# Performance work log

Hardware: AMD Instinct MI355X
Metric: run time of the kernel (lower is better)

The kernel has to match this reference:

```python
import jax, jax.numpy as jnp
import numpy as np

K = 16
BN_EPS = 1e-3  # keras BatchNormalization default epsilon
LRELU_ALPHA = 0.1


def _lrelu(x):
    return jnp.where(x > 0, x, LRELU_ALPHA * x)


def _bn(x, gamma, beta):
    # training-mode batch norm over all axes except the last (channels)
    axes = tuple(range(x.ndim - 1))
    m = jnp.mean(x, axis=axes)
    v = jnp.var(x, axis=axes)
    return gamma * (x - m) * jax.lax.rsqrt(v + BN_EPS) + beta


def setup_inputs() -> dict:
    key = jax.random.key(0)
    ks = jax.random.split(key, 14)
    N, P, Cp, C0 = 32, 1024, 3, 64
    channels = [128, 128, 256]
    inp = {
        "points": jax.random.normal(ks[0], (N, P, Cp), dtype=jnp.float32),
        "features": jax.random.normal(ks[1], (N, P, C0), dtype=jnp.float32),
    }
    # edge-conv 1x1 weights (no bias, with_bn=True); glorot-ish scaling
    c_in = 2 * C0
    for i, c_out in enumerate(channels):
        scale = (2.0 / (c_in + c_out)) ** 0.5
        inp[f"W{i}"] = jax.random.normal(ks[2 + i], (c_in, c_out), dtype=jnp.float32) * scale
        inp[f"g{i}"] = jnp.ones((c_out,), dtype=jnp.float32)
        inp[f"b{i}"] = jnp.zeros((c_out,), dtype=jnp.float32)
        c_in = c_out
    # shortcut 1x1 conv C0 -> channels[-1]
    scale = (2.0 / (C0 + channels[-1])) ** 0.5
    inp["Wsc"] = jax.random.normal(ks[10], (C0, channels[-1]), dtype=jnp.float32) * scale
    inp["gsc"] = jnp.ones((channels[-1],), dtype=jnp.float32)
    inp["bsc"] = jnp.zeros((channels[-1],), dtype=jnp.float32)
    return inp


def reference(points, features, W0, g0, b0, W1, g1, b1, W2, g2, b2, Wsc, gsc, bsc):
    # pairwise squared distance matrix D: (N, P, P)
    r = jnp.sum(points * points, axis=-1)
    D = r[:, :, None] - 2.0 * jnp.einsum("npc,nqc->npq", points, points) + r[:, None, :]
    # kNN indices, excluding self (first neighbor)
    _, idx = jax.lax.top_k(-D, K + 1)
    idx = idx[:, :, 1:]  # (N, P, K)
    # gather neighbor features per batch element -> (N, P, K, C0)
    knn_fts = jax.vmap(lambda f, i: f[i])(features, idx)
    center = jnp.broadcast_to(features[:, :, None, :], knn_fts.shape)
    x = jnp.concatenate([center, knn_fts - center], axis=-1)  # (N, P, K, 2*C0)
    for W, g, b in ((W0, g0, b0), (W1, g1, b1), (W2, g2, b2)):
        x = _lrelu(_bn(jnp.einsum("npkc,cd->npkd", x, W), g, b))
    fts = jnp.mean(x, axis=2)  # average pooling over K -> (N, P, C_out)
    sc = _bn(jnp.einsum("npc,cd->npd", features, Wsc), gsc, bsc)
    return _lrelu(sc + fts)
```

## Files before the change

### kernel.cpp

```cpp
#include <hip/hip_runtime.h>
#include <stdint.h>

typedef __bf16 bf16x8 __attribute__((ext_vector_type(8)));
typedef float f32x4 __attribute__((ext_vector_type(4)));

union FragU { uint4 q; bf16x8 v; };

__device__ __forceinline__ float bf2f(uint32_t h){
  union U{uint32_t u; float f;} x; x.u = h<<16; return x.f;
}
__device__ __forceinline__ uint32_t f2bf(float f){
  union U{float f; uint32_t u;} x; x.f=f;
  return (x.u + 0x7FFFu + ((x.u>>16)&1u)) >> 16;
}
__device__ __forceinline__ float lrelu(float x){ return fmaxf(x, 0.1f*x); }

__global__ __launch_bounds__(256) void knn_kernel(const float* __restrict__ points, int* __restrict__ idx){
  __shared__ float sx[1024], sy[1024], sz[1024];
  __shared__ unsigned long long scand[4][64];
  const int n = blockIdx.y;
  const float* P = points + (size_t)n*1024*3;
  for(int q=threadIdx.x; q<1024; q+=256){
    sx[q]=P[q*3+0]; sy[q]=P[q*3+1]; sz[q]=P[q*3+2];
  }
  __syncthreads();
  const int wv = threadIdx.x>>6;
  const int lane = threadIdx.x & 63;
  const int p = blockIdx.x*4 + wv;
  const double px=sx[p], py=sy[p], pz=sz[p];
  const double rp = px*px+py*py+pz*pz;
  unsigned long long e[16];
  const int prel = p - lane;
  #pragma unroll
  for(int j=0;j<16;j++){
    const int q = lane + j*64;
    double qx=sx[q], qy=sy[q], qz=sz[q];
    double rq = qx*qx+qy*qy+qz*qz;
    double dot = px*qx+py*qy+pz*qz;
    float key = fmaxf((float)((rp+rq) - 2.0*dot), 0.0f);
    if(prel == j*64) key = __builtin_inff();
    e[j] = ((unsigned long long)__float_as_uint(key) << 10) | (unsigned)q;
  }
  unsigned long long h = e[0];
  #pragma unroll
  for(int j=1;j<16;j++) h = (e[j] < h) ? e[j] : h;
  {
    unsigned long long hs = h;
    #pragma unroll
    for(int k=2;k<=64;k<<=1){
      #pragma unroll
      for(int j=32;j>0;j>>=1){
        if(j < k){
          unsigned long long o = __shfl_xor(hs, j);
          const bool keepMax = (((lane & j)!=0) ^ ((lane & k)!=0));
          hs = keepMax ? (hs > o ? hs : o) : (hs < o ? hs : o);
        }
      }
    }
    h = hs;
  }
  const unsigned long long H = __shfl(h, 15);
  int cnt = 0;
  #pragma unroll
  for(int j=0;j<16;j++) cnt += (e[j] <= H) ? 1 : 0;
  int inc = cnt;
  #pragma unroll
  for(int d=1; d<64; d<<=1){
    int t = __shfl_up(inc, d);
    if(lane >= d) inc += t;
  }
  const int m = __shfl(inc, 63);
  const int base = inc - cnt;
  int* op = idx + ((size_t)n*1024 + p)*16;
  if(m <= 64){
    unsigned long long* sc = scand[wv];
    int slot = base;
    #pragma unroll
    for(int j=0;j<16;j++){
      if(e[j] <= H){ sc[slot] = e[j]; slot++; }
    }
    unsigned long long v = (lane < m) ? sc[lane] : ~0ULL;
    #pragma unroll
    for(int k=2;k<=64;k<<=1){
      #pragma unroll
      for(int j=32;j>0;j>>=1){
        if(j < k){
          unsigned long long o = __shfl_xor(v, j);
          const bool keepMax = (((lane & j)!=0) ^ ((lane & k)!=0));
          v = keepMax ? (v > o ? v : o) : (v < o ? v : o);
        }
      }
    }
    if(lane < 16) op[lane] = (int)(v & 1023u);
  } else {
    for(int it=0; it<16; ++it){
      unsigned long long bd = e[0];
      #pragma unroll
      for(int j=1;j<16;j++) bd = (e[j] < bd) ? e[j] : bd;
      unsigned long long pk = bd;
      #pragma unroll
      for(int s=1;s<64;s<<=1){
        unsigned long long o = __shfl_xor(pk, s);
        pk = (o < pk) ? o : pk;
      }
      #pragma unroll
      for(int j=0;j<16;j++) e[j] = (e[j]==pk) ? ~0ULL : e[j];
      if(lane==0) op[it] = (int)(pk & 1023u);
    }
  }
}

__global__ void wprep_kernel(const float* __restrict__ W0, const float* __restrict__ Wsc,
                             const float* __restrict__ W1, const float* __restrict__ W2,
                             uint16_t* __restrict__ Wpp, uint16_t* __restrict__ W1p,
                             uint16_t* __restrict__ W2p){
  const int stride = gridDim.x*blockDim.x;
  const int t0 = blockIdx.x*blockDim.x + threadIdx.x;
  for(int o=t0; o<32768; o+=stride){
    int j=o&7, l=(o>>3)&63, kc=(o>>9)&1, ct=(o>>10)&3, w=o>>12;
    int k = kc*32 + (l>>4)*8 + j;
    int c = w*64 + ct*16 + (l&15);
    float val;
    if(c<128)      val = W0[k*128+c] - W0[(k+64)*128+c];
    else if(c<256) val = W0[(k+64)*128 + (c-128)];
    else           val = Wsc[k*256 + (c-256)];
    Wpp[o] = (uint16_t)f2bf(val);
  }
  for(int o=t0; o<16384; o+=stride){
    int j=o&7, l=(o>>3)&63, kc=(o>>9)&3, ct=(o>>11)&1, w=o>>12;
    int k = kc*32 + (l>>4)*8 + j, c = w*32 + ct*16 + (l&15);
    W1p[o] = (uint16_t)f2bf(W1[k*128+c]);
  }
  for(int o=t0; o<32768; o+=stride){
    int j=o&7, l=(o>>3)&63, kc=(o>>9)&3, ct=(o>>11)&3, w=o>>13;
    int k = kc*32 + (l>>4)*8 + j, c = w*64 + ct*16 + (l&15);
    W2p[o] = (uint16_t)f2bf(W2[k*256+c]);
  }
}

__global__ __launch_bounds__(512) void proj_kernel(const float* __restrict__ feat,
    const uint16_t* __restrict__ Wpp,
    float* __restrict__ F1, float* __restrict__ F2, float* __restrict__ Fsc,
    float* __restrict__ screps){
  __shared__ alignas(16) uint16_t sA[64*64];
  const int b = blockIdx.x;
  const int tid = threadIdx.x;
  {
    const int row = tid>>3, cc = tid&7;
    const float* src = feat + ((size_t)b*64+row)*64 + cc*8;
    const float4 f0 = *(const float4*)(src);
    const float4 f1 = *(const float4*)(src+4);
    uint32_t pk[4] = { f2bf(f0.x)|(f2bf(f0.y)<<16), f2bf(f0.z)|(f2bf(f0.w)<<16),
                       f2bf(f1.x)|(f2bf(f1.y)<<16), f2bf(f1.z)|(f2bf(f1.w)<<16) };
    int bo = row*128 + cc*16; bo ^= (row&7)<<4;
    *(uint4*)((char*)sA + bo) = make_uint4(pk[0],pk[1],pk[2],pk[3]);
  }
  __syncthreads();
  const int w = tid>>6, l = tid&63;
  FragU bfr[4][2];
  #pragma unroll
  for(int ct=0;ct<4;ct++)
    #pragma unroll
    for(int kc=0;kc<2;kc++)
      bfr[ct][kc].q = *(const uint4*)(Wpp + ((size_t)((w*4+ct)*2+kc))*512 + l*8);
  f32x4 acc[4][4] = {};
  #pragma unroll
  for(int rt=0;rt<4;rt++){
    FragU a[2];
    #pragma unroll
    for(int kc=0;kc<2;kc++){
      const int row = rt*16 + (l&15);
      int bo = row*128 + kc*64 + (l>>4)*16; bo ^= (row&7)<<4;
      a[kc].q = *(const uint4*)((const char*)sA + bo);
    }
    #pragma unroll
    for(int ct=0;ct<4;ct++)
      #pragma unroll
      for(int kc=0;kc<2;kc++)
        acc[rt][ct] = __builtin_amdgcn_mfma_f32_16x16x32_bf16(a[kc].v, bfr[ct][kc].v, acc[rt][ct], 0,0,0);
  }
  #pragma unroll
  for(int rt=0;rt<4;rt++){
    #pragma unroll
    for(int ct=0;ct<4;ct++){
      const int c = w*64 + ct*16 + (l&15);
      const int rowg = b*64 + rt*16 + (l>>4)*4;
      #pragma unroll
      for(int reg=0;reg<4;reg++){
        float v = acc[rt][ct][reg];
        if(c < 128)      F1[(size_t)(rowg+reg)*128 + c] = v;
        else if(c < 256) F2[(size_t)(rowg+reg)*128 + (c-128)] = v;
        else             Fsc[(size_t)(rowg+reg)*256 + (c-256)] = v;
      }
    }
  }
  if(w>=4){
    #pragma unroll
    for(int ct=0;ct<4;ct++){
      float s=0.f, sq=0.f;
      #pragma unroll
      for(int rt=0;rt<4;rt++)
        #pragma unroll
        for(int reg=0;reg<4;reg++){ float v=acc[rt][ct][reg]; s+=v; sq+=v*v; }
      s += __shfl_xor(s,16); sq += __shfl_xor(sq,16);
      s += __shfl_xor(s,32); sq += __shfl_xor(sq,32);
      if(l<16){
        const int c = (w-4)*64 + ct*16 + l;
        atomicAdd(&screps[((b&31)*2+0)*256 + c], s);
        atomicAdd(&screps[((b&31)*2+1)*256 + c], sq);
      }
    }
  }
}

__global__ __launch_bounds__(256) void y0stats_kernel(const float* __restrict__ F1,
    const float* __restrict__ F2, const int* __restrict__ idx, float* __restrict__ reps){
  __shared__ int sIdx[256];
  const int tid = threadIdx.x;
  const int r0 = blockIdx.x*256;
  sIdx[tid] = idx[r0 + tid];
  __syncthreads();
  const int cg = tid & 31;
  const int rs = tid >> 5;
  const int nbase = (r0 >> 14) << 10;
  f32x4 s = {0,0,0,0}, sq = {0,0,0,0};
  for(int rr=0; rr<32; rr+=4){
    #pragma unroll
    for(int u=0;u<4;u++){
      const int r = rs*32 + rr + u;
      const int np = (r0 + r) >> 4;
      const int g = sIdx[r];
      const float4 a = *(const float4*)(F1 + (size_t)np*128 + cg*4);
      const float4 c = *(const float4*)(F2 + (size_t)(nbase + g)*128 + cg*4);
      float v0=a.x+c.x, v1=a.y+c.y, v2=a.z+c.z, v3=a.w+c.w;
      s[0]+=v0; s[1]+=v1; s[2]+=v2; s[3]+=v3;
      sq[0]+=v0*v0; sq[1]+=v1*v1; sq[2]+=v2*v2; sq[3]+=v3*v3;
    }
  }
  #pragma unroll
  for(int e=0;e<4;e++){
    s[e]  += __shfl_xor(s[e], 32);
    sq[e] += __shfl_xor(sq[e], 32);
  }
  if((tid&63) < 32){
    const int rep = blockIdx.x & 31;
    #pragma unroll
    for(int e=0;e<4;e++){
      atomicAdd(&reps[(rep*2+0)*128 + cg*4+e], s[e]);
      atomicAdd(&reps[(rep*2+1)*128 + cg*4+e], sq[e]);
    }
  }
}

__global__ void finalize_kernel(const float* __restrict__ reps, const float* __restrict__ gamma,
    const float* __restrict__ beta, float* __restrict__ s, float* __restrict__ t,
    int C, float inv_cnt){
  int c = threadIdx.x;
  if(c>=C) return;
  float sum=0.f, sq=0.f;
  for(int r2=0;r2<32;r2++){ sum += reps[(r2*2+0)*C + c]; sq += reps[(r2*2+1)*C + c]; }
  float m = sum*inv_cnt;
  float var = sq*inv_cnt - m*m;
  float sc = gamma[c]*rsqrtf(var + 1e-3f);
  s[c]=sc; t[c]=beta[c] - m*sc;
}

__global__ __launch_bounds__(256) void layer1_kernel(
    const float* __restrict__ F1, const float* __restrict__ F2, const int* __restrict__ idx,
    const uint16_t* __restrict__ W1p, const float* __restrict__ s0, const float* __restrict__ t0,
    uint16_t* __restrict__ y1, float* __restrict__ reps1){
  __shared__ alignas(16) uint16_t sA[64*128];
  __shared__ int sIdx[64];
  const int b = blockIdx.x;
  const int tid = threadIdx.x;
  if(tid < 64) sIdx[tid] = idx[b*64 + tid];
  const int row0 = tid>>4, q = tid&15;
  const float4 sc0a = *(const float4*)(s0 + q*8);
  const float4 sc0b = *(const float4*)(s0 + q*8 + 4);
  const float4 tt0a = *(const float4*)(t0 + q*8);
  const float4 tt0b = *(const float4*)(t0 + q*8 + 4);
  const int wv = tid>>6, l = tid&63;
  FragU bfr[2][4];
  #pragma unroll
  for(int ct=0;ct<2;ct++)
    #pragma unroll
    for(int kc=0;kc<4;kc++)
      bfr[ct][kc].q = *(const uint4*)(W1p + ((size_t)((wv*2+ct)*4+kc))*512 + l*8);
  __syncthreads();
  {
    const int npb = b*4;
    const int nbase = (b >> 8) << 10;
    int gg[4];
    #pragma unroll
    for(int jj=0;jj<4;jj++) gg[jj] = sIdx[row0 + jj*16];
    float4 va[4][4];
    #pragma unroll
    for(int jj=0;jj<4;jj++){
      const int np = npb + jj;
      const float* pf1 = F1 + (size_t)np*128 + q*8;
      const float* pf2 = F2 + (size_t)(nbase + gg[jj])*128 + q*8;
      va[jj][0] = *(const float4*)(pf1);
      va[jj][1] = *(const float4*)(pf1+4);
      va[jj][2] = *(const float4*)(pf2);
      va[jj][3] = *(const float4*)(pf2+4);
    }
    #pragma unroll
    for(int jj=0;jj<4;jj++){
      const int rw = row0 + jj*16;
      float v[8] = {va[jj][0].x+va[jj][2].x, va[jj][0].y+va[jj][2].y,
                    va[jj][0].z+va[jj][2].z, va[jj][0].w+va[jj][2].w,
                    va[jj][1].x+va[jj][3].x, va[jj][1].y+va[jj][3].y,
                    va[jj][1].z+va[jj][3].z, va[jj][1].w+va[jj][3].w};
      const float sc[8] = {sc0a.x,sc0a.y,sc0a.z,sc0a.w, sc0b.x,sc0b.y,sc0b.z,sc0b.w};
      const float tt[8] = {tt0a.x,tt0a.y,tt0a.z,tt0a.w, tt0b.x,tt0b.y,tt0b.z,tt0b.w};
      uint32_t pk[4];
      #pragma unroll
      for(int e=0;e<4;e++){
        float x0 = lrelu(sc[e*2]*v[e*2] + tt[e*2]);
        float x1 = lrelu(sc[e*2+1]*v[e*2+1] + tt[e*2+1]);
        pk[e] = f2bf(x0) | (f2bf(x1)<<16);
      }
      int bo = rw*256 + q*16; bo ^= (rw&7)<<4;
      *(uint4*)((char*)sA + bo) = make_uint4(pk[0],pk[1],pk[2],pk[3]);
    }
  }
  __syncthreads();
  f32x4 acc[4][2] = {};
  #pragma unroll
  for(int rt=0;rt<4;rt++){
    FragU a[4];
    #pragma unroll
    for(int kc=0;kc<4;kc++){
      const int rw = rt*16 + (l&15);
      int bo = rw*256 + kc*64 + (l>>4)*16; bo ^= (rw&7)<<4;
      a[kc].q = *(const uint4*)((const char*)sA + bo);
    }
    #pragma unroll
    for(int ct=0;ct<2;ct++)
      #pragma unroll
      for(int kc=0;kc<4;kc++)
        acc[rt][ct] = __builtin_amdgcn_mfma_f32_16x16x32_bf16(a[kc].v, bfr[ct][kc].v, acc[rt][ct], 0,0,0);
  }
  float ss[2]={0.f,0.f}, sq[2]={0.f,0.f};
  #pragma unroll
  for(int rt=0;rt<4;rt++)
    #pragma unroll
    for(int ct=0;ct<2;ct++)
      #pragma unroll
      for(int reg=0;reg<4;reg++){
        float v = acc[rt][ct][reg];
        ss[ct]+=v; sq[ct]+=v*v;
        const int CI = ((rt*4+wv)*2+ct)*4+reg;
        y1[(size_t)b*8192 + CI*64 + l] = (uint16_t)f2bf(v);
      }
  #pragma unroll
  for(int ct=0;ct<2;ct++){
    float a=ss[ct], b2=sq[ct];
    a += __shfl_xor(a,16); b2 += __shfl_xor(b2,16);
    a += __shfl_xor(a,32); b2 += __shfl_xor(b2,32);
    if((l>>4)==0){
      const int c = wv*32 + ct*16 + l;
      atomicAdd(&reps1[((b&31)*2+0)*128 + c], a);
      atomicAdd(&reps1[((b&31)*2+1)*128 + c], b2);
    }
  }
}

template<int FINAL>
__global__ __launch_bounds__(512, 4) void layer2_kernel(
    const uint16_t* __restrict__ y1, const uint16_t* __restrict__ W2p,
    const float* __restrict__ s1, const float* __restrict__ t1,
    float* __restrict__ reps2,
    const float* __restrict__ s2, const float* __restrict__ t2,
    const float* __restrict__ Fsc, const float* __restrict__ ssc, const float* __restrict__ tsc,
    float* __restrict__ out){
  __shared__ alignas(16) uint16_t sA[2][8192];
  __shared__ float sBN[256];
  const int tid = threadIdx.x;
  const int w = tid>>6, l = tid&63;
  if(tid<128){ sBN[tid]=s1[tid]; sBN[128+tid]=t1[tid]; }
  FragU bfr[2][4];
  #pragma unroll
  for(int ct=0;ct<2;ct++)
    #pragma unroll
    for(int kc=0;kc<4;kc++)
      bfr[ct][kc].q = *(const uint4*)(W2p + ((size_t)((w*2+ct)*4+kc))*512 + l*8);
  int uc0[2], ubo[2];
  #pragma unroll
  for(int k=0;k<2;k++){
    const int u = tid + k*512;
    const int l8 = u&7, CI = u>>3;
    const int reg = CI&3, ct = (CI>>2)&1, w8 = (CI>>3)&3, rt = CI>>5;
    const int row = rt*16 + (l8>>1)*4 + reg;
    const int c0 = w8*32 + ct*16 + (l8&1)*8;
    uc0[k] = c0;
    ubo[k] = (row*256 + c0*2) ^ ((row&7)<<4);
  }
  float sc2v[2], tt2v[2], sscv[2], tscv[2];
  if(FINAL){
    #pragma unroll
    for(int ct=0;ct<2;ct++){
      const int c = w*32 + ct*16 + (l&15);
      sc2v[ct]=s2[c]; tt2v[ct]=t2[c]; sscv[ct]=ssc[c]; tscv[ct]=tsc[c];
    }
  }
  const int bt0 = blockIdx.x*16;
  uint4 va[2];
  #pragma unroll
  for(int k=0;k<2;k++)
    va[k] = *(const uint4*)(y1 + (size_t)bt0*8192 + (size_t)(tid+k*512)*8);
  __syncthreads();
  #pragma unroll
  for(int k=0;k<2;k++){
    const float4 sa = *(const float4*)(&sBN[uc0[k]]);
    const float4 sb = *(const float4*)(&sBN[uc0[k]+4]);
    const float4 ta = *(const float4*)(&sBN[128+uc0[k]]);
    const float4 tb = *(const float4*)(&sBN[128+uc0[k]+4]);
    const float scv[8]={sa.x,sa.y,sa.z,sa.w, sb.x,sb.y,sb.z,sb.w};
    const float ttv[8]={ta.x,ta.y,ta.z,ta.w, tb.x,tb.y,tb.z,tb.w};
    const uint32_t e[4] = {va[k].x, va[k].y, va[k].z, va[k].w};
    uint32_t pk[4];
    #pragma unroll
    for(int j=0;j<4;j++){
      float x0 = lrelu(scv[j*2]*bf2f(e[j]&0xffffu) + ttv[j*2]);
      float x1 = lrelu(scv[j*2+1]*bf2f(e[j]>>16) + ttv[j*2+1]);
      pk[j] = f2bf(x0) | (f2bf(x1)<<16);
    }
    *(uint4*)((char*)sA[0] + ubo[k]) = make_uint4(pk[0],pk[1],pk[2],pk[3]);
  }
  __syncthreads();
  float ssA[2]={0,0}, sqA[2]={0,0};
  for(int t=0; t<16; ++t){
    const int bt = bt0 + t;
    const int p = t&1;
    if(t<15){
      #pragma unroll
      for(int k=0;k<2;k++)
        va[k] = *(const uint4*)(y1 + (size_t)(bt+1)*8192 + (size_t)(tid+k*512)*8);
    }
    f32x4 acc[4][2] = {};
    #pragma unroll
    for(int rt=0;rt<4;rt++){
      FragU a[4];
      #pragma unroll
      for(int kc=0;kc<4;kc++){
        const int rw = rt*16 + (l&15);
        int bo = rw*256 + kc*64 + (l>>4)*16; bo ^= (rw&7)<<4;
        a[kc].q = *(const uint4*)((const char*)sA[p] + bo);
      }
      #pragma unroll
      for(int ct=0;ct<2;ct++)
        #pragma unroll
        for(int kc=0;kc<4;kc++)
          acc[rt][ct] = __builtin_amdgcn_mfma_f32_16x16x32_bf16(a[kc].v, bfr[ct][kc].v, acc[rt][ct], 0,0,0);
    }
    if(FINAL==0){
      #pragma unroll
      for(int ct=0;ct<2;ct++)
        #pragma unroll
        for(int rt=0;rt<4;rt++)
          #pragma unroll
          for(int reg=0;reg<4;reg++){
            float v = acc[rt][ct][reg];
            ssA[ct]+=v; sqA[ct]+=v*v;
          }
    } else {
      #pragma unroll
      for(int rt=0;rt<4;rt++){
        const int np = bt*4 + rt;
        #pragma unroll
        for(int ct=0;ct<2;ct++){
          const int c = w*32 + ct*16 + (l&15);
          float s=0.f;
          #pragma unroll
          for(int reg=0;reg<4;reg++) s += lrelu(sc2v[ct]*acc[rt][ct][reg] + tt2v[ct]);
          s += __shfl_xor(s,16);
          s += __shfl_xor(s,32);
          if((l>>4)==0){
            float fts = s*(1.0f/16.0f);
            float sc = sscv[ct]*Fsc[(size_t)np*256+c] + tscv[ct];
            out[(size_t)np*256+c] = lrelu(sc + fts);
          }
        }
      }
    }
    if(t<15){
      #pragma unroll
      for(int k=0;k<2;k++){
        const float4 sa = *(const float4*)(&sBN[uc0[k]]);
        const float4 sb = *(const float4*)(&sBN[uc0[k]+4]);
        const float4 ta = *(const float4*)(&sBN[128+uc0[k]]);
        const float4 tb = *(const float4*)(&sBN[128+uc0[k]+4]);
        const float scv[8]={sa.x,sa.y,sa.z,sa.w, sb.x,sb.y,sb.z,sb.w};
        const float ttv[8]={ta.x,ta.y,ta.z,ta.w, tb.x,tb.y,tb.z,tb.w};
        const uint32_t e[4] = {va[k].x, va[k].y, va[k].z, va[k].w};
        uint32_t pk[4];
        #pragma unroll
        for(int j=0;j<4;j++){
          float x0 = lrelu(scv[j*2]*bf2f(e[j]&0xffffu) + ttv[j*2]);
          float x1 = lrelu(scv[j*2+1]*bf2f(e[j]>>16) + ttv[j*2+1]);
          pk[j] = f2bf(x0) | (f2bf(x1)<<16);
        }
        *(uint4*)((char*)sA[p^1] + ubo[k]) = make_uint4(pk[0],pk[1],pk[2],pk[3]);
      }
    }
    __syncthreads();
  }
  if(FINAL==0){
    #pragma unroll
    for(int ct=0;ct<2;ct++){
      float a=ssA[ct], b2=sqA[ct];
      a += __shfl_xor(a,16); b2 += __shfl_xor(b2,16);
      a += __shfl_xor(a,32); b2 += __shfl_xor(b2,32);
      if((l>>4)==0){
        const int c = w*32 + ct*16 + l;
        const int rep = blockIdx.x & 31;
        atomicAdd(&reps2[(rep*2+0)*256 + c], a);
        atomicAdd(&reps2[(rep*2+1)*256 + c], b2);
      }
    }
  }
}

extern "C" void kernel_launch(void* const* d_in, const int* in_sizes, int n_in,
                              void* d_out, int out_size, void* d_ws, size_t ws_size,
                              hipStream_t stream) {
  const float* points   = (const float*)d_in[0];
  const float* features = (const float*)d_in[1];
  const float* W0  = (const float*)d_in[2];
  const float* g0  = (const float*)d_in[3];
  const float* b0  = (const float*)d_in[4];
  const float* W1  = (const float*)d_in[5];
  const float* g1  = (const float*)d_in[6];
  const float* b1  = (const float*)d_in[7];
  const float* W2  = (const float*)d_in[8];
  const float* g2  = (const float*)d_in[9];
  const float* b2  = (const float*)d_in[10];
  const float* Wsc = (const float*)d_in[11];
  const float* gsc = (const float*)d_in[12];
  const float* bsc = (const float*)d_in[13];
  float* out = (float*)d_out;

  float* ws = (float*)d_ws;
  size_t off = 0;
  float* screps = ws + off; off += 16384;
  float* reps0  = ws + off; off += 8192;
  float* reps1  = ws + off; off += 8192;
  float* reps2  = ws + off; off += 16384;
  float* ssc = ws + off; off += 256;
  float* tsc = ws + off; off += 256;
  float* s0  = ws + off; off += 128;
  float* t0  = ws + off; off += 128;
  float* s1v = ws + off; off += 128;
  float* t1v = ws + off; off += 128;
  float* s2v = ws + off; off += 256;
  float* t2v = ws + off; off += 256;
  int*   idxb = (int*)(ws + off); off += 524288;
  float* F1  = ws + off; off += (size_t)32768*128;
  float* F2  = ws + off; off += (size_t)32768*128;
  float* Fsc = ws + off; off += (size_t)32768*256;
  uint16_t* W1p = (uint16_t*)(ws + off); off += 8192;
  uint16_t* W2p = (uint16_t*)(ws + off); off += 16384;
  uint16_t* Wpp = (uint16_t*)(ws + off); off += 16384;
  uint16_t* y1  = (uint16_t*)(ws + off); off += (size_t)33554432;

  hipMemsetAsync(d_ws, 0, 49152*sizeof(float), stream);

  knn_kernel<<<dim3(256,32), 256, 0, stream>>>(points, idxb);
  wprep_kernel<<<128, 256, 0, stream>>>(W0, Wsc, W1, W2, Wpp, W1p, W2p);
  proj_kernel<<<512, 512, 0, stream>>>(features, Wpp, F1, F2, Fsc, screps);
  finalize_kernel<<<1, 256, 0, stream>>>(screps, gsc, bsc, ssc, tsc, 256, 1.0f/32768.0f);
  y0stats_kernel<<<2048, 256, 0, stream>>>(F1, F2, idxb, reps0);
  finalize_kernel<<<1, 128, 0, stream>>>(reps0, g0, b0, s0, t0, 128, 1.0f/524288.0f);
  layer1_kernel<<<8192, 256, 0, stream>>>(F1, F2, idxb, W1p, s0, t0, y1, reps1);
  finalize_kernel<<<1, 128, 0, stream>>>(reps1, g1, b1, s1v, t1v, 128, 1.0f/524288.0f);
  layer2_kernel<0><<<512, 512, 0, stream>>>(y1, W2p, s1v, t1v, reps2,
                                            nullptr, nullptr, nullptr, nullptr, nullptr, nullptr);
  finalize_kernel<<<1, 256, 0, stream>>>(reps2, g2, b2, s2v, t2v, 256, 1.0f/524288.0f);
  layer2_kernel<1><<<512, 512, 0, stream>>>(y1, W2p, s1v, t1v, nullptr,
                                            s2v, t2v, Fsc, ssc, tsc, out);
}
```

Before: 299.7 us.

## Write BN1-activated fragments back in place for direct LDS loads in final pass

The stats pass of layer 2 now writes the BN1+LeakyReLU-activated bf16 A fragments back into y1, in place and in MFMA fragment order, using wave 0 only. The final pass then reads these pre-activated fragments with global_load_lds straight into shared memory. This removes the repeated BN1 normalization, the bf16 unpack/repack and the register staging from the final pass, and its LDS reads become linear. In exchange the stats pass adds 64MB of global writes, and correctness relies on each block's in-place overwrite touching only tiles that block has already loaded.

```diff
diff --git a/kernel.cpp b/kernel.cpp
--- a/kernel.cpp
+++ b/kernel.cpp
@@ -366,14 +366,10 @@
   }
 }
 
-template<int FINAL>
-__global__ __launch_bounds__(512, 4) void layer2_kernel(
-    const uint16_t* __restrict__ y1, const uint16_t* __restrict__ W2p,
+__global__ __launch_bounds__(512, 4) void layer2s_kernel(
+    uint16_t* __restrict__ y1, const uint16_t* __restrict__ W2p,
     const float* __restrict__ s1, const float* __restrict__ t1,
-    float* __restrict__ reps2,
-    const float* __restrict__ s2, const float* __restrict__ t2,
-    const float* __restrict__ Fsc, const float* __restrict__ ssc, const float* __restrict__ tsc,
-    float* __restrict__ out){
+    float* __restrict__ reps2){
   __shared__ alignas(16) uint16_t sA[2][8192];
   __shared__ float sBN[256];
   const int tid = threadIdx.x;
@@ -395,14 +391,6 @@
     const int c0 = w8*32 + ct*16 + (l8&1)*8;
     uc0[k] = c0;
     ubo[k] = (row*256 + c0*2) ^ ((row&7)<<4);
-  }
-  float sc2v[2], tt2v[2], sscv[2], tscv[2];
-  if(FINAL){
-    #pragma unroll
-    for(int ct=0;ct<2;ct++){
-      const int c = w*32 + ct*16 + (l&15);
-      sc2v[ct]=s2[c]; tt2v[ct]=t2[c]; sscv[ct]=ssc[c]; tscv[ct]=tsc[c];
-    }
   }
   const int bt0 = blockIdx.x*16;
   uint4 va[2];
@@ -448,42 +436,26 @@
         int bo = rw*256 + kc*64 + (l>>4)*16; bo ^= (rw&7)<<4;
         a[kc].q = *(const uint4*)((const char*)sA[p] + bo);
       }
+      if(w==0){
+        #pragma unroll
+        for(int kc=0;kc<4;kc++)
+          *(uint4*)(y1 + (size_t)bt*8192 + (size_t)((rt*4+kc)*64 + l)*8) = a[kc].q;
+      }
       #pragma unroll
       for(int ct=0;ct<2;ct++)
         #pragma unroll
         for(int kc=0;kc<4;kc++)
           acc[rt][ct] = __builtin_amdgcn_mfma_f32_16x16x32_bf16(a[kc].v, bfr[ct][kc].v, acc[rt][ct], 0,0,0);
     }
-    if(FINAL==0){
-      #pragma unroll
-      for(int ct=0;ct<2;ct++)
+    #pragma unroll
+    for(int ct=0;ct<2;ct++)
+      #pragma unroll
+      for(int rt=0;rt<4;rt++)
         #pragma unroll
-        for(int rt=0;rt<4;rt++)
-          #pragma unroll
-          for(int reg=0;reg<4;reg++){
-            float v = acc[rt][ct][reg];
-            ssA[ct]+=v; sqA[ct]+=v*v;
-          }
-    } else {
-      #pragma unroll
-      for(int rt=0;rt<4;rt++){
-        const int np = bt*4 + rt;
-        #pragma unroll
-        for(int ct=0;ct<2;ct++){
-          const int c = w*32 + ct*16 + (l&15);
-          float s=0.f;
-          #pragma unroll
-          for(int reg=0;reg<4;reg++) s += lrelu(sc2v[ct]*acc[rt][ct][reg] + tt2v[ct]);
-          s += __shfl_xor(s,16);
-          s += __shfl_xor(s,32);
-          if((l>>4)==0){
-            float fts = s*(1.0f/16.0f);
-            float sc = sscv[ct]*Fsc[(size_t)np*256+c] + tscv[ct];
-            out[(size_t)np*256+c] = lrelu(sc + fts);
-          }
+        for(int reg=0;reg<4;reg++){
+          float v = acc[rt][ct][reg];
+          ssA[ct]+=v; sqA[ct]+=v*v;
         }
-      }
-    }
     if(t<15){
       #pragma unroll
       for(int k=0;k<2;k++){
@@ -506,19 +478,87 @@
     }
     __syncthreads();
   }
-  if(FINAL==0){
-    #pragma unroll
-    for(int ct=0;ct<2;ct++){
-      float a=ssA[ct], b2=sqA[ct];
-      a += __shfl_xor(a,16); b2 += __shfl_xor(b2,16);
-      a += __shfl_xor(a,32); b2 += __shfl_xor(b2,32);
-      if((l>>4)==0){
-        const int c = w*32 + ct*16 + l;
-        const int rep = blockIdx.x & 31;
-        atomicAdd(&reps2[(rep*2+0)*256 + c], a);
-        atomicAdd(&reps2[(rep*2+1)*256 + c], b2);
-      }
-    }
+  #pragma unroll
+  for(int ct=0;ct<2;ct++){
+    float a=ssA[ct], b2=sqA[ct];
+    a += __shfl_xor(a,16); b2 += __shfl_xor(b2,16);
+    a += __shfl_xor(a,32); b2 += __shfl_xor(b2,32);
+    if((l>>4)==0){
+      const int c = w*32 + ct*16 + l;
+      const int rep = blockIdx.x & 31;
+      atomicAdd(&reps2[(rep*2+0)*256 + c], a);
+      atomicAdd(&reps2[(rep*2+1)*256 + c], b2);
+    }
+  }
+}
+
+__global__ __launch_bounds__(512, 4) void layer2f_kernel(
+    const uint16_t* __restrict__ y1b, const uint16_t* __restrict__ W2p,
+    const float* __restrict__ s2, const float* __restrict__ t2,
+    const float* __restrict__ Fsc, const float* __restrict__ ssc, const float* __restrict__ tsc,
+    float* __restrict__ out){
+  __shared__ alignas(16) uint16_t sA[2][8192];
+  const int tid = threadIdx.x;
+  const int w = tid>>6, l = tid&63;
+  FragU bfr[2][4];
+  #pragma unroll
+  for(int ct=0;ct<2;ct++)
+    #pragma unroll
+    for(int kc=0;kc<4;kc++)
+      bfr[ct][kc].q = *(const uint4*)(W2p + ((size_t)((w*2+ct)*4+kc))*512 + l*8);
+  float sc2v[2], tt2v[2], sscv[2], tscv[2];
+  #pragma unroll
+  for(int ct=0;ct<2;ct++){
+    const int c = w*32 + ct*16 + (l&15);
+    sc2v[ct]=s2[c]; tt2v[ct]=t2[c]; sscv[ct]=ssc[c]; tscv[ct]=tsc[c];
+  }
+  const int bt0 = blockIdx.x*16;
+  {
+    const uint16_t* gp = y1b + (size_t)bt0*8192 + w*512 + l*8;
+    __builtin_amdgcn_global_load_lds((const uint32_t*)gp,        (uint32_t*)&sA[0][w*512 + l*8],        16, 0, 0);
+    __builtin_amdgcn_global_load_lds((const uint32_t*)(gp+4096), (uint32_t*)&sA[0][4096 + w*512 + l*8], 16, 0, 0);
+  }
+  __syncthreads();
+  for(int t=0; t<16; ++t){
+    const int bt = bt0 + t;
+    const int p = t&1;
+    if(t<15){
+      const uint16_t* gp = y1b + (size_t)(bt+1)*8192 + w*512 + l*8;
+      __builtin_amdgcn_global_load_lds((const uint32_t*)gp,        (uint32_t*)&sA[p^1][w*512 + l*8],        16, 0, 0);
+      __builtin_amdgcn_global_load_lds((const uint32_t*)(gp+4096), (uint32_t*)&sA[p^1][4096 + w*512 + l*8], 16, 0, 0);
+    }
+    f32x4 acc[4][2] = {};
+    #pragma unroll
+    for(int rt=0;rt<4;rt++){
+      FragU a[4];
+      #pragma unroll
+      for(int kc=0;kc<4;kc++)
+        a[kc].q = *(const uint4*)((const char*)sA[p] + (size_t)((rt*4+kc)*64 + l)*16);
+      #pragma unroll
+      for(int ct=0;ct<2;ct++)
+        #pragma unroll
+        for(int kc=0;kc<4;kc++)
+          acc[rt][ct] = __builtin_amdgcn_mfma_f32_16x16x32_bf16(a[kc].v, bfr[ct][kc].v, acc[rt][ct], 0,0,0);
+    }
+    #pragma unroll
+    for(int rt=0;rt<4;rt++){
+      const int np = bt*4 + rt;
+      #pragma unroll
+      for(int ct=0;ct<2;ct++){
+        const int c = w*32 + ct*16 + (l&15);
+        float s=0.f;
+        #pragma unroll
+        for(int reg=0;reg<4;reg++) s += lrelu(sc2v[ct]*acc[rt][ct][reg] + tt2v[ct]);
+        s += __shfl_xor(s,16);
+        s += __shfl_xor(s,32);
+        if((l>>4)==0){
+          float fts = s*(1.0f/16.0f);
+          float sc = sscv[ct]*Fsc[(size_t)np*256+c] + tscv[ct];
+          out[(size_t)np*256+c] = lrelu(sc + fts);
+        }
+      }
+    }
+    __syncthreads();
   }
 }
 
@@ -574,9 +614,7 @@
   finalize_kernel<<<1, 128, 0, stream>>>(reps0, g0, b0, s0, t0, 128, 1.0f/524288.0f);
   layer1_kernel<<<8192, 256, 0, stream>>>(F1, F2, idxb, W1p, s0, t0, y1, reps1);
   finalize_kernel<<<1, 128, 0, stream>>>(reps1, g1, b1, s1v, t1v, 128, 1.0f/524288.0f);
-  layer2_kernel<0><<<512, 512, 0, stream>>>(y1, W2p, s1v, t1v, reps2,
-                                            nullptr, nullptr, nullptr, nullptr, nullptr, nullptr);
+  layer2s_kernel<<<512, 512, 0, stream>>>(y1, W2p, s1v, t1v, reps2);
   finalize_kernel<<<1, 256, 0, stream>>>(reps2, g2, b2, s2v, t2v, 256, 1.0f/524288.0f);
-  layer2_kernel<1><<<512, 512, 0, stream>>>(y1, W2p, s1v, t1v, nullptr,
-                                            s2v, t2v, Fsc, ssc, tsc, out);
-}
+  layer2f_kernel<<<512, 512, 0, stream>>>(y1, W2p, s2v, t2v, Fsc, ssc, tsc, out);
+}
```

After: 298.1 us. Within noise of the previous version (-0.5%).
